# Performance work log

Hardware: AMD Instinct MI355X
Metric: run time of the kernel (lower is better)

The kernel has to match this reference:

```python
import jax, jax.numpy as jnp
import numpy as np
import math

B, C, IMG_H, IMG_W = 64, 3, 224, 224
P = 14                 # patches per side
PH = PW = 16           # patch size
D = 768                # hidden_d (= C*PH*PW = input_d)
L = 12                 # n_blocks
NH = 12                # n_heads
DH = D // NH           # d_head = 64
FF = 4 * D             # mlp hidden
S = P * P + 1          # 197 tokens (cls + patches)
EXTRACT = (2, 5, 8, 11)
LN_EPS = 1e-5


def _sinusoidal_pos(seq_len, d):
    pos = np.arange(seq_len, dtype=np.float32)[:, None]
    div = np.exp(np.arange(0, d, 2, dtype=np.float32) * -(math.log(10000.0) / d))
    out = np.zeros((seq_len, d), dtype=np.float32)
    out[:, 0::2] = np.sin(pos * div)
    out[:, 1::2] = np.cos(pos * div)
    return jnp.asarray(out)


def setup_inputs() -> dict:
    key = jax.random.key(0)
    ks = jax.random.split(key, 12)
    sc = 0.02
    return {
        "images": jax.random.normal(ks[0], (B, C, IMG_H, IMG_W), jnp.float32),
        "mapper_w": jax.random.normal(ks[1], (D, D), jnp.float32) * sc,  # input_d == D
        "mapper_b": jnp.zeros((D,), jnp.float32),
        "cls_token": jax.random.uniform(ks[2], (1, D), jnp.float32),
        "pos_emb": _sinusoidal_pos(S, D),
        "ln1_g": jnp.ones((L, D), jnp.float32),
        "ln1_b": jnp.zeros((L, D), jnp.float32),
        "qw": jax.random.normal(ks[3], (L, NH, DH, DH), jnp.float32) * sc,
        "qb": jnp.zeros((L, NH, DH), jnp.float32),
        "kw": jax.random.normal(ks[4], (L, NH, DH, DH), jnp.float32) * sc,
        "kb": jnp.zeros((L, NH, DH), jnp.float32),
        "vw": jax.random.normal(ks[5], (L, NH, DH, DH), jnp.float32) * sc,
        "vb": jnp.zeros((L, NH, DH), jnp.float32),
        "ow": jax.random.normal(ks[6], (L, D, D), jnp.float32) * sc,
        "ob": jnp.zeros((L, D), jnp.float32),
        "ln2_g": jnp.ones((L, D), jnp.float32),
        "ln2_b": jnp.zeros((L, D), jnp.float32),
        "mlp_w1": jax.random.normal(ks[7], (L, FF, D), jnp.float32) * sc,
        "mlp_b1": jnp.zeros((L, FF), jnp.float32),
        "mlp_w2": jax.random.normal(ks[8], (L, D, FF), jnp.float32) * sc,
        "mlp_b2": jnp.zeros((L, D), jnp.float32),
    }


def _layernorm(x, g, b):
    mu = jnp.mean(x, axis=-1, keepdims=True)
    var = jnp.mean(jnp.square(x - mu), axis=-1, keepdims=True)
    return (x - mu) * jax.lax.rsqrt(var + LN_EPS) * g + b


def reference(images, mapper_w, mapper_b, cls_token, pos_emb,
              ln1_g, ln1_b, qw, qb, kw, kb, vw, vb, ow, ob,
              ln2_g, ln2_b, mlp_w1, mlp_b1, mlp_w2, mlp_b2):
    n = images.shape[0]
    # patchify: [n,C,H,W] -> [n, P*P, C*PH*PW]
    patches = images.reshape(n, C, P, PH, P, PW)
    patches = patches.transpose(0, 2, 4, 1, 3, 5).reshape(n, P * P, C * PH * PW)
    tokens = patches @ mapper_w.T + mapper_b                      # [n, P*P, D]
    cls = jnp.broadcast_to(cls_token[None], (n, 1, D))
    x = jnp.concatenate([cls, tokens], axis=1) + pos_emb[None]    # [n, S, D]

    extracted = []
    for i in range(L):
        # --- MHSA (note: scale is d_head**2, as in the source) ---
        h = _layernorm(x, ln1_g[i], ln1_b[i])
        hh = h.reshape(n, S, NH, DH)
        q = jnp.einsum('bshd,hed->bshe', hh, qw[i]) + qb[i]
        k = jnp.einsum('bshd,hed->bshe', hh, kw[i]) + kb[i]
        v = jnp.einsum('bshd,hed->bshe', hh, vw[i]) + vb[i]
        scores = jnp.einsum('bqhe,bkhe->bhqk', q, k) / (DH ** 2)
        attn = jax.nn.softmax(scores, axis=-1)
        ctx = jnp.einsum('bhqk,bkhe->bqhe', attn, v).reshape(n, S, D)
        x = x + ctx @ ow[i].T + ob[i]
        # --- MLP ---
        h2 = _layernorm(x, ln2_g[i], ln2_b[i])
        mid = jax.nn.gelu(h2 @ mlp_w1[i].T + mlp_b1[i], approximate=False)
        x = x + mid @ mlp_w2[i].T + mlp_b2[i]
        if i in EXTRACT:
            extracted.append(x)
    return jnp.stack(extracted)  # [4, n, S, D]
```

## Files before the change

### kernel.cpp

```cpp
#include <hip/hip_runtime.h>
#include <hip/hip_bf16.h>
#include <math.h>

static constexpr int NB   = 64;
static constexpr int SS   = 197;
static constexpr int DD   = 768;
static constexpr int NHH  = 12;
static constexpr int DHH  = 64;
static constexpr int FFF  = 3072;
static constexpr int TOK  = NB * SS;
static constexpr int NPAT = 196;
static constexpr int PADM = 12672;
static constexpr int PADM2= 12800;
static constexpr long NX  = (long)TOK * DD;
static constexpr int APAD = 256;

typedef __attribute__((ext_vector_type(8))) short bf16x8;
typedef __attribute__((ext_vector_type(4))) float f32x4;

__device__ inline void gll16(const __hip_bfloat16* g, __hip_bfloat16* l) {
    __builtin_amdgcn_global_load_lds(
        (const __attribute__((address_space(1))) void*)g,
        (__attribute__((address_space(3))) void*)l, 16, 0, 0);
}

template<int EPI, bool OUTBF>
__global__ __launch_bounds__(256, 4) void gemm128(
    const __hip_bfloat16* __restrict__ A, int lda,
    const __hip_bfloat16* __restrict__ Bt, int ldb,
    void* __restrict__ Cout, int ldc,
    const float* __restrict__ bias,
    const float* __restrict__ Rm, int ldr,
    float* __restrict__ out2,
    int M, int N, int K)
{
    __shared__ __hip_bfloat16 sh[3][2][128 * 32];

    const int nbx = gridDim.x;
    const int nwg = nbx * gridDim.y;
    int flat = blockIdx.y * nbx + blockIdx.x;
    {
        int q = nwg >> 3, r = nwg & 7;
        int xcd = flat & 7, idx = flat >> 3;
        flat = (xcd < r ? xcd * (q + 1) : r * (q + 1) + (xcd - r) * q) + idx;
    }
    const int m0 = (flat / nbx) * 128;
    const int n0 = (flat % nbx) * 128;

    const int t = threadIdx.x;
    const int wid = t >> 6, lane = t & 63;
    const int wm = wid >> 1, wn = wid & 1;
    const int l15 = lane & 15, g0 = lane >> 4;
    const int rcol = ((g0 ^ ((l15 >> 1) & 3)) * 8);

    const int srl = t >> 2, sg = t & 3;

    auto stage = [&](int buf, int k0) {
        #pragma unroll
        for (int j = 0; j < 2; ++j) {
            int row = j * 64 + srl;
            int gs = sg ^ ((row >> 1) & 3);
            gll16(A + (long)(m0 + row) * lda + k0 + gs * 8,
                  &sh[buf][0][row * 32 + sg * 8]);
        }
        #pragma unroll
        for (int j = 0; j < 2; ++j) {
            int row = j * 64 + srl;
            int gs = sg ^ ((row >> 1) & 3);
            gll16(Bt + (long)(n0 + row) * ldb + k0 + gs * 8,
                  &sh[buf][1][row * 32 + sg * 8]);
        }
    };

    f32x4 acc[4][4] = {};
    const int NT = K >> 5;

    stage(0, 0);
    stage(1, 32);
    asm volatile("s_waitcnt vmcnt(4)" ::: "memory");
    __builtin_amdgcn_sched_barrier(0);
    __builtin_amdgcn_s_barrier();
    __builtin_amdgcn_sched_barrier(0);

    int cur = 0;
    for (int kt = 0; kt < NT; ++kt) {
        const bool st2 = (kt + 2 < NT);
        const bool w1n = (kt + 1 < NT);
        int stbuf = cur + 2; if (stbuf >= 3) stbuf -= 3;

        bf16x8 af[4], bfr[4];
        #pragma unroll
        for (int mi = 0; mi < 4; ++mi)
            af[mi] = *reinterpret_cast<const bf16x8*>(
                &sh[cur][0][(wm * 64 + mi * 16 + l15) * 32 + rcol]);
        #pragma unroll
        for (int ni = 0; ni < 4; ++ni)
            bfr[ni] = *reinterpret_cast<const bf16x8*>(
                &sh[cur][1][(wn * 64 + ni * 16 + l15) * 32 + rcol]);

        if (st2) stage(stbuf, (kt + 2) << 5);

        asm volatile("s_waitcnt lgkmcnt(0)" ::: "memory");
        __builtin_amdgcn_sched_barrier(0);
        __builtin_amdgcn_s_setprio(1);
        #pragma unroll
        for (int mi = 0; mi < 4; ++mi)
            #pragma unroll
            for (int ni = 0; ni < 4; ++ni)
                acc[mi][ni] = __builtin_amdgcn_mfma_f32_16x16x32_bf16(
                    af[mi], bfr[ni], acc[mi][ni], 0, 0, 0);
        __builtin_amdgcn_s_setprio(0);
        __builtin_amdgcn_sched_barrier(0);
        if (st2)      { asm volatile("s_waitcnt vmcnt(4)" ::: "memory"); }
        else if (w1n) { asm volatile("s_waitcnt vmcnt(0)" ::: "memory"); }
        __builtin_amdgcn_sched_barrier(0);
        __builtin_amdgcn_s_barrier();
        __builtin_amdgcn_sched_barrier(0);

        cur = (cur == 2) ? 0 : cur + 1;
    }

    #pragma unroll
    for (int mi = 0; mi < 4; ++mi) {
        #pragma unroll
        for (int r = 0; r < 4; ++r) {
            int gm = m0 + wm * 64 + mi * 16 + (lane >> 4) * 4 + r;
            if (gm >= M) continue;
            #pragma unroll
            for (int ni = 0; ni < 4; ++ni) {
                int gn = n0 + wn * 64 + ni * 16 + (lane & 15);
                float v = acc[mi][ni][r];
                if (bias) v += bias[gn];
                if (EPI == 1) v += Rm[(long)gm * ldr + gn];
                if (EPI == 2) v = 0.5f * v * (1.0f + erff(v * 0.70710678118654752f));
                if (OUTBF) {
                    ((__hip_bfloat16*)Cout)[(long)gm * ldc + gn] = __float2bfloat16(v);
                } else {
                    ((float*)Cout)[(long)gm * ldc + gn] = v;
                    if (EPI == 1 && out2) out2[(long)gm * ldc + gn] = v;
                }
            }
        }
    }
}

__global__ __launch_bounds__(256) void gemm_qkv(
    const __hip_bfloat16* __restrict__ A, int lda, long sAlo,
    const __hip_bfloat16* __restrict__ Bt, int ldb, long sBhi,
    const float* __restrict__ bias, long sbhi,
    __hip_bfloat16* __restrict__ qb_, __hip_bfloat16* __restrict__ kb_,
    __hip_bfloat16* __restrict__ vtb,
    int M, int N, int K)
{
    __shared__ __hip_bfloat16 As[128 * 64];
    __shared__ __hip_bfloat16 Bs[128 * 64];

    const int zz = blockIdx.z;
    A  += zz * sAlo;
    Bt += zz * sBhi;
    bias += zz * sbhi;

    const int t = threadIdx.x;
    const int wid = t >> 6, lane = t & 63;
    const int wm = wid >> 1, wn = wid & 1;
    const int m0 = blockIdx.y * 128, n0 = blockIdx.x * 128;

    const int srow = t >> 3;
    const int scol = (t & 7) * 8;

    f32x4 acc[4][4] = {};

    for (int k0 = 0; k0 < K; k0 += 64) {
        #pragma unroll
        for (int i = 0; i < 4; ++i) {
            const __hip_bfloat16* ga = A + (long)(m0 + i * 32 + srow) * lda + k0 + scol;
            __hip_bfloat16* la = As + (i * 256 + wid * 64) * 8;
            gll16(ga, la);
            const __hip_bfloat16* gb = Bt + (long)(n0 + i * 32 + srow) * ldb + k0 + scol;
            __hip_bfloat16* lb = Bs + (i * 256 + wid * 64) * 8;
            gll16(gb, lb);
        }
        asm volatile("s_waitcnt vmcnt(0)" ::: "memory");
        __syncthreads();

        #pragma unroll
        for (int kk = 0; kk < 2; ++kk) {
            bf16x8 af[4], bfr[4];
            #pragma unroll
            for (int mi = 0; mi < 4; ++mi)
                af[mi] = *reinterpret_cast<const bf16x8*>(
                    &As[(wm * 64 + mi * 16 + (lane & 15)) * 64 + kk * 32 + (lane >> 4) * 8]);
            #pragma unroll
            for (int ni = 0; ni < 4; ++ni)
                bfr[ni] = *reinterpret_cast<const bf16x8*>(
                    &Bs[(wn * 64 + ni * 16 + (lane & 15)) * 64 + kk * 32 + (lane >> 4) * 8]);
            #pragma unroll
            for (int mi = 0; mi < 4; ++mi)
                #pragma unroll
                for (int ni = 0; ni < 4; ++ni)
                    acc[mi][ni] = __builtin_amdgcn_mfma_f32_16x16x32_bf16(
                        af[mi], bfr[ni], acc[mi][ni], 0, 0, 0);
        }
        __syncthreads();
    }

    #pragma unroll
    for (int mi = 0; mi < 4; ++mi) {
        #pragma unroll
        for (int r = 0; r < 4; ++r) {
            int gm = m0 + wm * 64 + mi * 16 + (lane >> 4) * 4 + r;
            if (gm >= M) continue;
            int bq = gm / 197, sq = gm - bq * 197;
            #pragma unroll
            for (int ni = 0; ni < 4; ++ni) {
                int gn = n0 + wn * 64 + ni * 16 + (lane & 15);
                if (gn >= N) continue;
                float v = acc[mi][ni][r] + bias[gn];
                int c = gn >> 6, e = gn & 63;
                __hip_bfloat16 bv = __float2bfloat16(v);
                if (c == 0)      qb_[(long)gm * DD + zz * 64 + e] = bv;
                else if (c == 1) kb_[(long)gm * DD + zz * 64 + e] = bv;
                else             vtb[(((long)(bq * NHH + zz)) * 128 + e) * APAD + sq] = bv;
            }
        }
    }
}

__global__ __launch_bounds__(256) void attn_flash(
    const __hip_bfloat16* __restrict__ qbuf,
    const __hip_bfloat16* __restrict__ kbuf,
    const __hip_bfloat16* __restrict__ vt,
    __hip_bfloat16* __restrict__ ctx)
{
    constexpr int KLD = 72;
    constexpr int VLD = 232;
    constexpr int PLD = 232;
    __shared__ __hip_bfloat16 Kl[208 * KLD];
    __shared__ __hip_bfloat16 Vl[64 * VLD];
    __shared__ __hip_bfloat16 Pl[4][16 * PLD];

    const int h = blockIdx.x, b = blockIdx.y;
    const int t = threadIdx.x;
    const int w = t >> 6, lane = t & 63;
    const int l15 = lane & 15, g0 = lane >> 4;

    const long row0 = (long)b * 197;
    const int  hc   = h * 64;

    for (int task = t; task < 208 * 8; task += 256) {
        int r = task >> 3, g = task & 7;
        float4 vv = *reinterpret_cast<const float4*>(kbuf + (row0 + r) * DD + hc + g * 8);
        *reinterpret_cast<float4*>(&Kl[r * KLD + g * 8]) = vv;
    }
    const __hip_bfloat16* vsrc0 = vt + (long)(b * NHH + h) * 128 * APAD;
    for (int task = t; task < 64 * 32; task += 256) {
        int e = task >> 5, g = task & 31;
        if (g < 28) {
            float4 vv = *reinterpret_cast<const float4*>(vsrc0 + (long)e * APAD + g * 8);
            *reinterpret_cast<float4*>(&Vl[e * VLD + g * 8]) = vv;
        }
    }
    __syncthreads();

    __hip_bfloat16* Pw = Pl[w];

    for (int qc = w; qc < 13; qc += 4) {
        const int q0 = qc * 16;

        const __hip_bfloat16* qsrc = qbuf + (row0 + q0 + l15) * DD + hc + g0 * 8;
        bf16x8 qf0 = *reinterpret_cast<const bf16x8*>(qsrc);
        bf16x8 qf1 = *reinterpret_cast<const bf16x8*>(qsrc + 32);

        f32x4 sacc[13];
        #pragma unroll
        for (int n = 0; n < 13; ++n) {
            bf16x8 kf0 = *reinterpret_cast<const bf16x8*>(&Kl[(n * 16 + l15) * KLD + g0 * 8]);
            bf16x8 kf1 = *reinterpret_cast<const bf16x8*>(&Kl[(n * 16 + l15) * KLD + 32 + g0 * 8]);
            f32x4 z = {0.f, 0.f, 0.f, 0.f};
            z = __builtin_amdgcn_mfma_f32_16x16x32_bf16(qf0, kf0, z, 0, 0, 0);
            sacc[n] = __builtin_amdgcn_mfma_f32_16x16x32_bf16(qf1, kf1, z, 0, 0, 0);
        }

        const int kcol = l15;
        float lrow[4];
        #pragma unroll
        for (int r = 0; r < 4; ++r) {
            float mx = -3.0e38f;
            #pragma unroll
            for (int n = 0; n < 13; ++n) {
                float s = sacc[n][r] * (1.0f / 4096.0f);
                if (n * 16 + kcol < 197) mx = fmaxf(mx, s);
            }
            #pragma unroll
            for (int off = 1; off < 16; off <<= 1) mx = fmaxf(mx, __shfl_xor(mx, off));
            float sum = 0.f;
            #pragma unroll
            for (int n = 0; n < 14; ++n) {
                float p = 0.f;
                if (n < 13 && n * 16 + kcol < 197) {
                    p = __expf(sacc[n][r] * (1.0f / 4096.0f) - mx);
                    sum += p;
                }
                Pw[(g0 * 4 + r) * PLD + n * 16 + kcol] = __float2bfloat16(p);
            }
            #pragma unroll
            for (int off = 1; off < 16; off <<= 1) sum += __shfl_xor(sum, off);
            lrow[r] = sum;
        }

        asm volatile("s_waitcnt lgkmcnt(0)" ::: "memory");

        f32x4 pv[4] = {};
        #pragma unroll
        for (int kc = 0; kc < 7; ++kc) {
            bf16x8 pf = *reinterpret_cast<const bf16x8*>(&Pw[l15 * PLD + kc * 32 + g0 * 8]);
            #pragma unroll
            for (int ni = 0; ni < 4; ++ni) {
                bf16x8 vf = *reinterpret_cast<const bf16x8*>(&Vl[(ni * 16 + l15) * VLD + kc * 32 + g0 * 8]);
                pv[ni] = __builtin_amdgcn_mfma_f32_16x16x32_bf16(pf, vf, pv[ni], 0, 0, 0);
            }
        }

        #pragma unroll
        for (int r = 0; r < 4; ++r) {
            int q = q0 + g0 * 4 + r;
            if (q >= 197) continue;
            float inv = 1.0f / lrow[r];
            #pragma unroll
            for (int ni = 0; ni < 4; ++ni)
                ctx[(row0 + q) * DD + hc + ni * 16 + l15] = __float2bfloat16(pv[ni][r] * inv);
        }
    }
}

__global__ __launch_bounds__(256) void ln_kernel(
    const float* __restrict__ X, const float* __restrict__ g,
    const float* __restrict__ b, __hip_bfloat16* __restrict__ H)
{
    const long row = blockIdx.x;
    const float* x = X + row * DD;
    const int t = threadIdx.x;
    float v[3];
    float s = 0.f, s2 = 0.f;
    #pragma unroll
    for (int i = 0; i < 3; ++i) {
        v[i] = x[t + i * 256];
        s += v[i]; s2 += v[i] * v[i];
    }
    #pragma unroll
    for (int off = 1; off < 64; off <<= 1) {
        s  += __shfl_xor(s,  off);
        s2 += __shfl_xor(s2, off);
    }
    __shared__ float red[2][4];
    const int lane = t & 63, w = t >> 6;
    if (lane == 0) { red[0][w] = s; red[1][w] = s2; }
    __syncthreads();
    float S1 = red[0][0] + red[0][1] + red[0][2] + red[0][3];
    float S2 = red[1][0] + red[1][1] + red[1][2] + red[1][3];
    float mu  = S1 * (1.0f / 768.0f);
    float var = S2 * (1.0f / 768.0f) - mu * mu;
    float rs  = rsqrtf(var + 1e-5f);
    __hip_bfloat16* h = H + row * DD;
    #pragma unroll
    for (int i = 0; i < 3; ++i) {
        int c = t + i * 256;
        h[c] = __float2bfloat16((v[i] - mu) * rs * g[c] + b[c]);
    }
}

__global__ void patchify_kernel(const float* __restrict__ img, __hip_bfloat16* __restrict__ patches)
{
    long idx = (long)blockIdx.x * 256 + threadIdx.x;
    const long total = (long)NB * NPAT * DD;
    if (idx >= total) return;
    int k  = (int)(idx % DD);
    long mp = idx / DD;
    int p  = (int)(mp % NPAT);
    long b = mp / NPAT;
    int c = k >> 8;
    int i = (k >> 4) & 15;
    int j = k & 15;
    int pr = p / 14, pc = p % 14;
    int hh = pr * 16 + i, ww = pc * 16 + j;
    patches[idx] = __float2bfloat16(img[((b * 3 + c) * 224 + hh) * 224 + ww]);
}

__global__ void assemble_kernel(const float* __restrict__ tok, const float* __restrict__ cls,
                                const float* __restrict__ pos, float* __restrict__ X)
{
    long idx = (long)blockIdx.x * 256 + threadIdx.x;
    if (idx >= NX) return;
    int d  = (int)(idx % DD);
    long bs = idx / DD;
    int s  = (int)(bs % SS);
    long b = bs / SS;
    float v = (s == 0) ? cls[d] : tok[(b * NPAT + s - 1) * DD + d];
    X[idx] = v + pos[(long)s * DD + d];
}

__global__ void f2b_kernel(const float* __restrict__ src, __hip_bfloat16* __restrict__ dst, long n4)
{
    long i = (long)blockIdx.x * 256 + threadIdx.x;
    if (i >= n4) return;
    float4 v = *reinterpret_cast<const float4*>(&src[i * 4]);
    __hip_bfloat16 o[4] = { __float2bfloat16(v.x), __float2bfloat16(v.y),
                            __float2bfloat16(v.z), __float2bfloat16(v.w) };
    *reinterpret_cast<uint2*>(&dst[i * 4]) = *reinterpret_cast<const uint2*>(o);
}

__global__ void f2b3_kernel(const float* __restrict__ s0, __hip_bfloat16* __restrict__ d0, long c0,
                            const float* __restrict__ s1, __hip_bfloat16* __restrict__ d1, long c1,
                            const float* __restrict__ s2, __hip_bfloat16* __restrict__ d2, long c2)
{
    long i = (long)blockIdx.x * 256 + threadIdx.x;
    const float* s; __hip_bfloat16* d;
    if (i < c0)                { s = s0; d = d0; }
    else if (i < c0 + c1)      { s = s1; d = d1; i -= c0; }
    else if (i < c0 + c1 + c2) { s = s2; d = d2; i -= c0 + c1; }
    else return;
    #pragma unroll
    for (int u = 0; u < 4; ++u) {
        float4 v = *reinterpret_cast<const float4*>(&s[i * 16 + u * 4]);
        __hip_bfloat16 o[4] = { __float2bfloat16(v.x), __float2bfloat16(v.y),
                                __float2bfloat16(v.z), __float2bfloat16(v.w) };
        *reinterpret_cast<uint2*>(&d[i * 16 + u * 4]) = *reinterpret_cast<const uint2*>(o);
    }
}

__global__ void qkvpack_kernel(const float* __restrict__ qw, const float* __restrict__ kw,
                               const float* __restrict__ vw, const float* __restrict__ qb,
                               const float* __restrict__ kb, const float* __restrict__ vb,
                               __hip_bfloat16* __restrict__ W, float* __restrict__ Bv)
{
    int idx = blockIdx.x * 256 + threadIdx.x;
    if (idx >= NHH * 192 * 64) return;
    int d = idx & 63;
    int rest = idx >> 6;
    int j = rest % 192;
    int h = rest / 192;
    int c = j >> 6, e = j & 63;
    const float* src = (c == 0 ? qw : c == 1 ? kw : vw) + ((long)h * 64 + e) * 64 + d;
    W[((long)h * 256 + j) * 64 + d] = __float2bfloat16(*src);
    if (d == 0) {
        const float* sb = (c == 0 ? qb : c == 1 ? kb : vb) + h * 64 + e;
        Bv[h * 192 + j] = *sb;
    }
}

extern "C" void kernel_launch(void* const* d_in, const int* in_sizes, int n_in,
                              void* d_out, int out_size, void* d_ws, size_t ws_size,
                              hipStream_t stream)
{
    const float* images   = (const float*)d_in[0];
    const float* mapper_w = (const float*)d_in[1];
    const float* mapper_b = (const float*)d_in[2];
    const float* cls      = (const float*)d_in[3];
    const float* pos      = (const float*)d_in[4];
    const float* ln1_g    = (const float*)d_in[5];
    const float* ln1_b    = (const float*)d_in[6];
    const float* qw       = (const float*)d_in[7];
    const float* qb       = (const float*)d_in[8];
    const float* kw       = (const float*)d_in[9];
    const float* kb       = (const float*)d_in[10];
    const float* vw       = (const float*)d_in[11];
    const float* vb       = (const float*)d_in[12];
    const float* ow       = (const float*)d_in[13];
    const float* ob       = (const float*)d_in[14];
    const float* ln2_g    = (const float*)d_in[15];
    const float* ln2_b    = (const float*)d_in[16];
    const float* w1       = (const float*)d_in[17];
    const float* b1       = (const float*)d_in[18];
    const float* w2       = (const float*)d_in[19];
    const float* b2       = (const float*)d_in[20];
    float* out = (float*)d_out;

    char* p0 = (char*)d_ws;
    char* pp = p0;
    auto alloc = [&](size_t bytes) { char* r = pp; pp += (bytes + 255) & ~(size_t)255; return r; };

    float*           x      = (float*)          alloc(NX * 4);
    __hip_bfloat16*  h16    = (__hip_bfloat16*) alloc((size_t)PADM2 * DD * 2);
    __hip_bfloat16*  ctx16  = (__hip_bfloat16*) alloc((size_t)PADM2 * DD * 2);
    __hip_bfloat16*  wbuf16 = (__hip_bfloat16*) alloc((size_t)(DD*DD + (size_t)FFF*DD*2) * 2);
    __hip_bfloat16*  wqkv16 = (__hip_bfloat16*) alloc((size_t)NHH * 256 * 64 * 2);
    float*           bqkv   = (float*)          alloc((size_t)NHH * 192 * 4);
    __hip_bfloat16*  qbuf   = (__hip_bfloat16*) alloc((size_t)PADM * DD * 2);
    __hip_bfloat16*  kbuf   = (__hip_bfloat16*) alloc((size_t)PADM * DD * 2);
    __hip_bfloat16*  vt     = (__hip_bfloat16*) alloc((size_t)NB * NHH * 128 * APAD * 2);
    char*            big    = alloc((size_t)PADM2 * FFF * 2);

    if ((size_t)(pp - p0) > ws_size) return;

    __hip_bfloat16* mid16     = (__hip_bfloat16*)big;
    __hip_bfloat16* patches16 = (__hip_bfloat16*)big;
    float*          tokens    = (float*)(big + (((size_t)NB * NPAT * DD * 2 + 255) & ~(size_t)255));

    __hip_bfloat16* ow16 = wbuf16;
    __hip_bfloat16* w116 = wbuf16 + (size_t)DD * DD;
    __hip_bfloat16* w216 = w116 + (size_t)FFF * DD;

    {
        long n = (long)NB * NPAT * DD;
        patchify_kernel<<<dim3((n + 255) / 256), dim3(256), 0, stream>>>(images, patches16);
        f2b_kernel<<<dim3((DD * DD / 4 + 255) / 256), dim3(256), 0, stream>>>(mapper_w, w116, DD * DD / 4);
        gemm128<0, false><<<dim3(DD / 128, (NB * NPAT) / 128), dim3(256), 0, stream>>>(
            patches16, DD, w116, DD, tokens, DD, mapper_b, nullptr, 0, nullptr,
            NB * NPAT, DD, DD);
        assemble_kernel<<<dim3((NX + 255) / 256), dim3(256), 0, stream>>>(tokens, cls, pos, x);
    }

    const int MT = (TOK + 127) / 128;
    const long C1 = (long)DD * DD / 16, C2 = (long)FFF * DD / 16;

    for (int l = 0; l < 12; ++l) {
        f2b3_kernel<<<dim3((int)((C1 + 2 * C2 + 255) / 256)), dim3(256), 0, stream>>>(
            ow + (long)l * DD * DD, ow16, C1,
            w1 + (long)l * FFF * DD, w116, C2,
            w2 + (long)l * FFF * DD, w216, C2);
        qkvpack_kernel<<<dim3((NHH * 192 * 64 + 255) / 256), dim3(256), 0, stream>>>(
            qw + (long)l * NHH * DHH * DHH, kw + (long)l * NHH * DHH * DHH,
            vw + (long)l * NHH * DHH * DHH,
            qb + (long)l * DD, kb + (long)l * DD, vb + (long)l * DD,
            wqkv16, bqkv);

        ln_kernel<<<dim3(TOK), dim3(256), 0, stream>>>(x, ln1_g + l * DD, ln1_b + l * DD, h16);

        gemm_qkv<<<dim3(2, MT, NHH), dim3(256), 0, stream>>>(
            h16, DD, 64,
            wqkv16, 64, (long)256 * 64,
            bqkv, 192,
            qbuf, kbuf, vt,
            TOK, 192, 64);

        attn_flash<<<dim3(NHH, NB), dim3(256), 0, stream>>>(qbuf, kbuf, vt, ctx16);

        gemm128<1, false><<<dim3(DD / 128, MT), dim3(256), 0, stream>>>(
            ctx16, DD, ow16, DD, x, DD, ob + l * DD, x, DD, nullptr,
            TOK, DD, DD);

        ln_kernel<<<dim3(TOK), dim3(256), 0, stream>>>(x, ln2_g + l * DD, ln2_b + l * DD, h16);

        gemm128<2, true><<<dim3(FFF / 128, MT), dim3(256), 0, stream>>>(
            h16, DD, w116, DD, mid16, FFF, b1 + l * FFF, nullptr, 0, nullptr,
            TOK, FFF, DD);

        int slot = (l == 2) ? 0 : (l == 5) ? 1 : (l == 8) ? 2 : (l == 11) ? 3 : -1;
        float* o2 = (slot >= 0) ? out + (long)slot * NX : nullptr;
        gemm128<1, false><<<dim3(DD / 128, MT), dim3(256), 0, stream>>>(
            mid16, FFF, w216, FFF, x, DD, b2 + l * DD, x, DD, o2,
            TOK, DD, FFF);
    }
}
```

Before: 5.580 ms.

## Add 256x128 pipelined GEMM for MLP up-projection and untranspose V storage

Adds a new 512-thread GEMM kernel with 256x128 tiles for the GELU MLP up-projection. It uses a K-step of 32, double-buffered direct-to-LDS loads with an XOR swizzle, XCD-aware workgroup remapping and MFMA priority boosting, aiming for better operand reuse and overlap of loads with compute. Separately, the QKV GEMM now writes V in the same row-major layout as Q and K instead of a strided transposed layout. The attention kernel transposes V while loading it into LDS and zero-fills the padding columns itself. This trades scattered global stores for scalar 2-byte LDS writes that may cause bank conflicts.

```diff
diff --git a/kernel.cpp b/kernel.cpp
--- a/kernel.cpp
+++ b/kernel.cpp
@@ -13,7 +13,6 @@
 static constexpr int PADM = 12672;
 static constexpr int PADM2= 12800;
 static constexpr long NX  = (long)TOK * DD;
-static constexpr int APAD = 256;
 
 typedef __attribute__((ext_vector_type(8))) short bf16x8;
 typedef __attribute__((ext_vector_type(4))) float f32x4;
@@ -144,12 +143,128 @@
     }
 }
 
+template<int EPI, bool OUTBF>
+__global__ __launch_bounds__(512, 6) void gemm256(
+    const __hip_bfloat16* __restrict__ A, int lda,
+    const __hip_bfloat16* __restrict__ Bt, int ldb,
+    void* __restrict__ Cout, int ldc,
+    const float* __restrict__ bias,
+    const float* __restrict__ Rm, int ldr,
+    float* __restrict__ out2,
+    int M, int N, int K)
+{
+    __shared__ __hip_bfloat16 sh[2][(256 + 128) * 32];
+
+    const int nbx = gridDim.x;
+    const int nwg = nbx * gridDim.y;
+    int flat = blockIdx.y * nbx + blockIdx.x;
+    {
+        int q = nwg >> 3, r = nwg & 7;
+        int xcd = flat & 7, idx = flat >> 3;
+        flat = (xcd < r ? xcd * (q + 1) : r * (q + 1) + (xcd - r) * q) + idx;
+    }
+    const int m0 = (flat / nbx) * 256;
+    const int n0 = (flat % nbx) * 128;
+
+    const int t = threadIdx.x;
+    const int wid = t >> 6, lane = t & 63;
+    const int wm = wid >> 1, wn = wid & 1;
+    const int l15 = lane & 15, g0 = lane >> 4;
+    const int rcol = ((g0 ^ ((l15 >> 1) & 3)) * 8);
+
+    const int srl = t >> 2, sg = t & 3;
+
+    auto stage = [&](int buf, int k0) {
+        #pragma unroll
+        for (int j = 0; j < 2; ++j) {
+            int row = j * 128 + srl;
+            int gs = sg ^ ((row >> 1) & 3);
+            gll16(A + (long)(m0 + row) * lda + k0 + gs * 8,
+                  &sh[buf][row * 32 + sg * 8]);
+        }
+        {
+            int gs = sg ^ ((srl >> 1) & 3);
+            gll16(Bt + (long)(n0 + srl) * ldb + k0 + gs * 8,
+                  &sh[buf][8192 + srl * 32 + sg * 8]);
+        }
+    };
+
+    f32x4 acc[4][4] = {};
+    const int NT = K >> 5;
+
+    stage(0, 0);
+    stage(1, 32);
+    asm volatile("s_waitcnt vmcnt(3)" ::: "memory");
+    __builtin_amdgcn_sched_barrier(0);
+    __builtin_amdgcn_s_barrier();
+    __builtin_amdgcn_sched_barrier(0);
+
+    for (int kt = 0; kt < NT; ++kt) {
+        const int cur = kt & 1;
+        const bool st2 = (kt + 2 < NT);
+        const bool w1n = (kt + 1 < NT);
+
+        bf16x8 af[4], bfr[4];
+        #pragma unroll
+        for (int mi = 0; mi < 4; ++mi)
+            af[mi] = *reinterpret_cast<const bf16x8*>(
+                &sh[cur][(wm * 64 + mi * 16 + l15) * 32 + rcol]);
+        #pragma unroll
+        for (int ni = 0; ni < 4; ++ni)
+            bfr[ni] = *reinterpret_cast<const bf16x8*>(
+                &sh[cur][8192 + (wn * 64 + ni * 16 + l15) * 32 + rcol]);
+        asm volatile("s_waitcnt lgkmcnt(0)" ::: "memory");
+        __builtin_amdgcn_sched_barrier(0);
+        __builtin_amdgcn_s_barrier();
+        __builtin_amdgcn_sched_barrier(0);
+
+        if (st2) stage(cur, (kt + 2) << 5);
+        __builtin_amdgcn_s_setprio(1);
+        #pragma unroll
+        for (int mi = 0; mi < 4; ++mi)
+            #pragma unroll
+            for (int ni = 0; ni < 4; ++ni)
+                acc[mi][ni] = __builtin_amdgcn_mfma_f32_16x16x32_bf16(
+                    af[mi], bfr[ni], acc[mi][ni], 0, 0, 0);
+        __builtin_amdgcn_s_setprio(0);
+        __builtin_amdgcn_sched_barrier(0);
+        if (st2)      { asm volatile("s_waitcnt vmcnt(3)" ::: "memory"); }
+        else if (w1n) { asm volatile("s_waitcnt vmcnt(0)" ::: "memory"); }
+        __builtin_amdgcn_sched_barrier(0);
+        __builtin_amdgcn_s_barrier();
+        __builtin_amdgcn_sched_barrier(0);
+    }
+
+    #pragma unroll
+    for (int mi = 0; mi < 4; ++mi) {
+        #pragma unroll
+        for (int r = 0; r < 4; ++r) {
+            int gm = m0 + wm * 64 + mi * 16 + (lane >> 4) * 4 + r;
+            if (gm >= M) continue;
+            #pragma unroll
+            for (int ni = 0; ni < 4; ++ni) {
+                int gn = n0 + wn * 64 + ni * 16 + (lane & 15);
+                float v = acc[mi][ni][r];
+                if (bias) v += bias[gn];
+                if (EPI == 1) v += Rm[(long)gm * ldr + gn];
+                if (EPI == 2) v = 0.5f * v * (1.0f + erff(v * 0.70710678118654752f));
+                if (OUTBF) {
+                    ((__hip_bfloat16*)Cout)[(long)gm * ldc + gn] = __float2bfloat16(v);
+                } else {
+                    ((float*)Cout)[(long)gm * ldc + gn] = v;
+                    if (EPI == 1 && out2) out2[(long)gm * ldc + gn] = v;
+                }
+            }
+        }
+    }
+}
+
 __global__ __launch_bounds__(256) void gemm_qkv(
     const __hip_bfloat16* __restrict__ A, int lda, long sAlo,
     const __hip_bfloat16* __restrict__ Bt, int ldb, long sBhi,
     const float* __restrict__ bias, long sbhi,
     __hip_bfloat16* __restrict__ qb_, __hip_bfloat16* __restrict__ kb_,
-    __hip_bfloat16* __restrict__ vtb,
+    __hip_bfloat16* __restrict__ vb_,
     int M, int N, int K)
 {
     __shared__ __hip_bfloat16 As[128 * 64];
@@ -210,7 +325,6 @@
         for (int r = 0; r < 4; ++r) {
             int gm = m0 + wm * 64 + mi * 16 + (lane >> 4) * 4 + r;
             if (gm >= M) continue;
-            int bq = gm / 197, sq = gm - bq * 197;
             #pragma unroll
             for (int ni = 0; ni < 4; ++ni) {
                 int gn = n0 + wn * 64 + ni * 16 + (lane & 15);
@@ -218,9 +332,8 @@
                 float v = acc[mi][ni][r] + bias[gn];
                 int c = gn >> 6, e = gn & 63;
                 __hip_bfloat16 bv = __float2bfloat16(v);
-                if (c == 0)      qb_[(long)gm * DD + zz * 64 + e] = bv;
-                else if (c == 1) kb_[(long)gm * DD + zz * 64 + e] = bv;
-                else             vtb[(((long)(bq * NHH + zz)) * 128 + e) * APAD + sq] = bv;
+                __hip_bfloat16* dst = (c == 0) ? qb_ : (c == 1) ? kb_ : vb_;
+                dst[(long)gm * DD + zz * 64 + e] = bv;
             }
         }
     }
@@ -229,7 +342,7 @@
 __global__ __launch_bounds__(256) void attn_flash(
     const __hip_bfloat16* __restrict__ qbuf,
     const __hip_bfloat16* __restrict__ kbuf,
-    const __hip_bfloat16* __restrict__ vt,
+    const __hip_bfloat16* __restrict__ vbuf,
     __hip_bfloat16* __restrict__ ctx)
 {
     constexpr int KLD = 72;
@@ -252,13 +365,18 @@
         float4 vv = *reinterpret_cast<const float4*>(kbuf + (row0 + r) * DD + hc + g * 8);
         *reinterpret_cast<float4*>(&Kl[r * KLD + g * 8]) = vv;
     }
-    const __hip_bfloat16* vsrc0 = vt + (long)(b * NHH + h) * 128 * APAD;
-    for (int task = t; task < 64 * 32; task += 256) {
-        int e = task >> 5, g = task & 31;
-        if (g < 28) {
-            float4 vv = *reinterpret_cast<const float4*>(vsrc0 + (long)e * APAD + g * 8);
-            *reinterpret_cast<float4*>(&Vl[e * VLD + g * 8]) = vv;
-        }
+    const __hip_bfloat16 bz = __float2bfloat16(0.0f);
+    for (int task = t; task < 64 * 27; task += 256) {
+        int e = task / 27, c = 197 + (task - e * 27);
+        Vl[e * VLD + c] = bz;
+    }
+    for (int task = t; task < 197 * 8; task += 256) {
+        int r = task >> 3, g = task & 7;
+        union { float4 f; __hip_bfloat16 hx[8]; } u;
+        u.f = *reinterpret_cast<const float4*>(vbuf + (row0 + r) * DD + hc + g * 8);
+        #pragma unroll
+        for (int j = 0; j < 8; ++j)
+            Vl[(g * 8 + j) * VLD + r] = u.hx[j];
     }
     __syncthreads();
 
@@ -487,7 +605,7 @@
     float*           bqkv   = (float*)          alloc((size_t)NHH * 192 * 4);
     __hip_bfloat16*  qbuf   = (__hip_bfloat16*) alloc((size_t)PADM * DD * 2);
     __hip_bfloat16*  kbuf   = (__hip_bfloat16*) alloc((size_t)PADM * DD * 2);
-    __hip_bfloat16*  vt     = (__hip_bfloat16*) alloc((size_t)NB * NHH * 128 * APAD * 2);
+    __hip_bfloat16*  vbuf   = (__hip_bfloat16*) alloc((size_t)PADM * DD * 2);
     char*            big    = alloc((size_t)PADM2 * FFF * 2);
 
     if ((size_t)(pp - p0) > ws_size) return;
@@ -510,7 +628,8 @@
         assemble_kernel<<<dim3((NX + 255) / 256), dim3(256), 0, stream>>>(tokens, cls, pos, x);
     }
 
-    const int MT = (TOK + 127) / 128;
+    const int MT  = (TOK + 127) / 128;
+    const int MT2 = (TOK + 255) / 256;
     const long C1 = (long)DD * DD / 16, C2 = (long)FFF * DD / 16;
 
     for (int l = 0; l < 12; ++l) {
@@ -530,10 +649,10 @@
             h16, DD, 64,
             wqkv16, 64, (long)256 * 64,
             bqkv, 192,
-            qbuf, kbuf, vt,
+            qbuf, kbuf, vbuf,
             TOK, 192, 64);
 
-        attn_flash<<<dim3(NHH, NB), dim3(256), 0, stream>>>(qbuf, kbuf, vt, ctx16);
+        attn_flash<<<dim3(NHH, NB), dim3(256), 0, stream>>>(qbuf, kbuf, vbuf, ctx16);
 
         gemm128<1, false><<<dim3(DD / 128, MT), dim3(256), 0, stream>>>(
             ctx16, DD, ow16, DD, x, DD, ob + l * DD, x, DD, nullptr,
@@ -541,7 +660,7 @@
 
         ln_kernel<<<dim3(TOK), dim3(256), 0, stream>>>(x, ln2_g + l * DD, ln2_b + l * DD, h16);
 
-        gemm128<2, true><<<dim3(FFF / 128, MT), dim3(256), 0, stream>>>(
+        gemm256<2, true><<<dim3(FFF / 128, MT2), dim3(512), 0, stream>>>(
             h16, DD, w116, DD, mid16, FFF, b1 + l * FFF, nullptr, 0, nullptr,
             TOK, FFF, DD);
 
```

Measured after the change: 12.20 ms. 2.19x slower.
